# Optimization experiments

Measured on AMD Instinct MI355X. Metric: run time of the kernel, lower is better.

## Reference

```python
import jax, jax.numpy as jnp
import numpy as np

DEPTH = 4
HEADS = 8
DIM = 512
MLP = 2048
EPS = 1e-5


def layernorm(x, w, b):
    m = x.mean(-1, keepdims=True)
    v = x.var(-1, keepdims=True)
    return (x - m) * jax.lax.rsqrt(v + EPS) * w + b


def setup_inputs() -> dict:
    key = jax.random.key(0)
    ks = jax.random.split(key, 6)
    s = 0.02
    x = jax.random.normal(ks[0], (4, 2048, DIM), dtype=jnp.float32)
    return {
        "x": x,
        "ln1_w": jnp.ones((DEPTH, DIM), jnp.float32),
        "ln1_b": jnp.zeros((DEPTH, DIM), jnp.float32),
        "qkv_w": jax.random.normal(ks[1], (DEPTH, 3 * DIM, DIM), jnp.float32) * s,
        "proj_w": jax.random.normal(ks[2], (DEPTH, DIM, DIM), jnp.float32) * s,
        "proj_b": jnp.zeros((DEPTH, DIM), jnp.float32),
        "ln2_w": jnp.ones((DEPTH, DIM), jnp.float32),
        "ln2_b": jnp.zeros((DEPTH, DIM), jnp.float32),
        "fc1_w": jax.random.normal(ks[3], (DEPTH, MLP, DIM), jnp.float32) * s,
        "fc1_b": jnp.zeros((DEPTH, MLP), jnp.float32),
        "fc2_w": jax.random.normal(ks[4], (DEPTH, DIM, MLP), jnp.float32) * s,
        "fc2_b": jnp.zeros((DEPTH, DIM), jnp.float32),
    }


def reference(x, ln1_w, ln1_b, qkv_w, proj_w, proj_b, ln2_w, ln2_b, fc1_w, fc1_b, fc2_w, fc2_b):
    B, N, C = x.shape
    Dh = C // HEADS
    scale = Dh ** (-0.5)
    for i in range(DEPTH):
        # PreNorm attention block
        h = layernorm(x, ln1_w[i], ln1_b[i])
        qkv = (h @ qkv_w[i].T).reshape(B, N, 3, HEADS, Dh).transpose(2, 0, 3, 1, 4)
        q, k, v = qkv[0], qkv[1], qkv[2]          # [B,H,N,Dh]
        attn = jax.nn.softmax(jnp.einsum('bhnd,bhmd->bhnm', q, k) * scale, axis=-1)
        o = jnp.einsum('bhnm,bhmd->bhnd', attn, v).transpose(0, 2, 1, 3).reshape(B, N, C)
        x = o @ proj_w[i].T + proj_b[i] + x
        # PreNorm FFN block (exact erf GELU, matching torch nn.GELU default)
        h = layernorm(x, ln2_w[i], ln2_b[i])
        h = jax.nn.gelu(h @ fc1_w[i].T + fc1_b[i], approximate=False)
        x = h @ fc2_w[i].T + fc2_b[i] + x
    return x
```

## Files before the change

### kernel.cpp

```cpp
#include <hip/hip_runtime.h>
#include <hip/hip_bf16.h>
#include <math.h>

#define NB 4
#define HEADS 8
#define DIM 512
#define MLP 2048
#define NT 2048
#define DH 64
#define M_TOK (NB*NT)

typedef __bf16 bf16;
typedef __bf16 bf16x2 __attribute__((ext_vector_type(2)));
typedef __bf16 bf16x4 __attribute__((ext_vector_type(4)));
typedef __bf16 bf16x8 __attribute__((ext_vector_type(8)));
typedef float f32x4 __attribute__((ext_vector_type(4)));

__device__ __forceinline__ void gl_lds16(const void* g, void* l) {
    __builtin_amdgcn_global_load_lds((const __attribute__((address_space(1))) unsigned int*)g,
                                     (__attribute__((address_space(3))) unsigned int*)l, 16, 0, 0);
}

#define BARRIER() do { __builtin_amdgcn_s_barrier(); asm volatile("" ::: "memory"); } while(0)
#define WAIT_VM4() asm volatile("s_waitcnt vmcnt(4)" ::: "memory")
#define WAIT_VM0() asm volatile("s_waitcnt vmcnt(0)" ::: "memory")

__global__ void cvt_bf16_kernel(const float* __restrict__ src, bf16* __restrict__ dst, int n) {
    int i = (blockIdx.x * 256 + threadIdx.x) * 4;
    if (i < n) {
        float4 v = *(const float4*)(src + i);
        bf16x4 o;
        o[0] = (bf16)v.x; o[1] = (bf16)v.y; o[2] = (bf16)v.z; o[3] = (bf16)v.w;
        *(bf16x4*)(dst + i) = o;
    }
}

__global__ void ln_kernel(const float* __restrict__ X, const float* __restrict__ gam,
                          const float* __restrict__ bet, bf16* __restrict__ out) {
    int w = threadIdx.x >> 6, l = threadIdx.x & 63;
    long row = (long)blockIdx.x * 4 + w;
    const float* xp = X + row * DIM + l * 8;
    float4 a = *(const float4*)xp;
    float4 b = *(const float4*)(xp + 4);
    float s1 = a.x + a.y + a.z + a.w + b.x + b.y + b.z + b.w;
    float s2 = a.x*a.x + a.y*a.y + a.z*a.z + a.w*a.w + b.x*b.x + b.y*b.y + b.z*b.z + b.w*b.w;
#pragma unroll
    for (int off = 32; off; off >>= 1) { s1 += __shfl_xor(s1, off); s2 += __shfl_xor(s2, off); }
    float mean = s1 * (1.f / 512.f);
    float var  = s2 * (1.f / 512.f) - mean * mean;
    float rstd = rsqrtf(var + 1e-5f);
    float4 g0 = *(const float4*)(gam + l * 8), g1 = *(const float4*)(gam + l * 8 + 4);
    float4 b0 = *(const float4*)(bet + l * 8), b1 = *(const float4*)(bet + l * 8 + 4);
    bf16x8 o;
    o[0] = (bf16)((a.x - mean) * rstd * g0.x + b0.x);
    o[1] = (bf16)((a.y - mean) * rstd * g0.y + b0.y);
    o[2] = (bf16)((a.z - mean) * rstd * g0.z + b0.z);
    o[3] = (bf16)((a.w - mean) * rstd * g0.w + b0.w);
    o[4] = (bf16)((b.x - mean) * rstd * g1.x + b1.x);
    o[5] = (bf16)((b.y - mean) * rstd * g1.y + b1.y);
    o[6] = (bf16)((b.z - mean) * rstd * g1.z + b1.z);
    o[7] = (bf16)((b.w - mean) * rstd * g1.w + b1.w);
    *(bf16x8*)(out + row * DIM + l * 8) = o;
}

#define G_LOADA(AF, B_, MQ) do { \
  _Pragma("unroll") for (int mi_ = 0; mi_ < 2; ++mi_) \
  _Pragma("unroll") for (int kk_ = 0; kk_ < 2; ++kk_) { \
    int row_ = wr * 64 + ((MQ) * 2 + mi_) * 16 + c; \
    AF[mi_][kk_] = *(const bf16x8*)&Abuf[B_][row_ * 64 + (((kk_ * 64 + g * 16) ^ sw) >> 1)]; \
  } } while (0)

#define G_LOADB(BF, B_, NQ) do { \
  _Pragma("unroll") for (int ni_ = 0; ni_ < 2; ++ni_) \
  _Pragma("unroll") for (int kk_ = 0; kk_ < 2; ++kk_) { \
    int row_ = wc * 64 + ((NQ) * 2 + ni_) * 16 + c; \
    BF[ni_][kk_] = *(const bf16x8*)&Bbuf[B_][row_ * 64 + (((kk_ * 64 + g * 16) ^ sw) >> 1)]; \
  } } while (0)

#define G_MFMA(AF, BF, MQ, NQ) do { \
  __builtin_amdgcn_s_setprio(1); \
  _Pragma("unroll") for (int mi_ = 0; mi_ < 2; ++mi_) \
  _Pragma("unroll") for (int ni_ = 0; ni_ < 2; ++ni_) \
  _Pragma("unroll") for (int kk_ = 0; kk_ < 2; ++kk_) \
    acc[(MQ)*2+mi_][(NQ)*2+ni_] = __builtin_amdgcn_mfma_f32_16x16x32_bf16( \
        AF[mi_][kk_], BF[ni_][kk_], acc[(MQ)*2+mi_][(NQ)*2+ni_], 0, 0, 0); \
  __builtin_amdgcn_s_setprio(0); \
} while (0)

#define G_STAGE_A(J_, H_) do { int j_ = (J_); if (j_ < nkt) { \
  bf16* db_ = Abuf[j_ & 1]; const bf16* sb_ = Aptr + (size_t)j_ * 64 + coloff; \
  _Pragma("unroll") for (int q_ = 0; q_ < 2; ++q_) { \
    int rw_ = q_ * 64 + (H_) * 32 + (w << 3); \
    gl_lds16(sb_ + (size_t)(arow0 + rw_ + lr) * KN, db_ + rw_ * 64); \
  } } } while (0)

#define G_STAGE_B(J_, H_) do { int j_ = (J_); if (j_ < nkt) { \
  bf16* db_ = Bbuf[j_ & 1]; const bf16* sb_ = Wptr + (size_t)j_ * 64 + coloff; \
  _Pragma("unroll") for (int q_ = 0; q_ < 2; ++q_) { \
    int rw_ = q_ * 64 + (H_) * 32 + (w << 3); \
    gl_lds16(sb_ + (size_t)(bcol0 + rw_ + lr) * KN, db_ + rw_ * 64); \
  } } } while (0)

template<int EPI, int KN>
__global__ __launch_bounds__(256, 2) void gemm128(const bf16* __restrict__ Aptr,
                                                  const bf16* __restrict__ Wptr,
                                                  const float* __restrict__ bias,
                                                  const float* __restrict__ resid,
                                                  void* outp, int N, bf16* __restrict__ vtout) {
    __shared__ bf16 Abuf[2][128 * 64];
    __shared__ bf16 Bbuf[2][128 * 64];
    const int t = threadIdx.x, w = t >> 6, l = t & 63;
    const int wr = w >> 1, wc = w & 1, g = l >> 4, c = l & 15;
    const int sw = (c & 7) << 4;
    const int lr = l >> 3;
    const int coloff = ((l & 7) ^ lr) << 3;

    int nwg = gridDim.x, bid = blockIdx.x;
    int q8 = nwg >> 3, r8 = nwg & 7;
    int xcd = bid & 7, rank = bid >> 3;
    int swz = (xcd < r8) ? xcd * (q8 + 1) + rank : r8 * (q8 + 1) + (xcd - r8) * q8 + rank;
    int tiles_n = N >> 7;
    long arow0 = (long)(swz / tiles_n) * 128;
    long bcol0 = (long)(swz % tiles_n) * 128;

    const int nkt = KN / 64;
    const int niter = nkt / 2;
    f32x4 acc[4][4] = {};
    bf16x8 af[2][2], bn0[2][2], bn1[2][2];

    G_STAGE_A(0, 0); G_STAGE_B(0, 0); G_STAGE_A(0, 1); G_STAGE_B(0, 1);
    G_STAGE_A(1, 0); G_STAGE_B(1, 0);

#pragma unroll 1
    for (int tt = 0; tt < niter; ++tt) {
        const int J0 = 2 * tt, J1 = 2 * tt + 1;
        const bool last = (tt == niter - 1);
        WAIT_VM4(); BARRIER();
        G_LOADA(af, 0, 0); G_LOADB(bn0, 0, 0);
        G_STAGE_A(J0 + 1, 1);
        G_MFMA(af, bn0, 0, 0);
        BARRIER();
        G_LOADB(bn1, 0, 1);
        G_STAGE_B(J0 + 1, 1);
        G_MFMA(af, bn1, 0, 1);
        BARRIER();
        G_LOADA(af, 0, 1);
        G_STAGE_A(J0 + 2, 0);
        G_MFMA(af, bn0, 1, 0);
        BARRIER();
        G_STAGE_B(J0 + 2, 0);
        G_MFMA(af, bn1, 1, 1);
        BARRIER();
        if (last) { WAIT_VM0(); } else { WAIT_VM4(); }
        BARRIER();
        G_LOADA(af, 1, 0); G_LOADB(bn0, 1, 0);
        G_STAGE_A(J1 + 1, 1);
        G_MFMA(af, bn0, 0, 0);
        BARRIER();
        G_LOADB(bn1, 1, 1);
        G_STAGE_B(J1 + 1, 1);
        G_MFMA(af, bn1, 0, 1);
        BARRIER();
        G_LOADA(af, 1, 1);
        G_STAGE_A(J1 + 2, 0);
        G_MFMA(af, bn0, 1, 0);
        BARRIER();
        G_STAGE_B(J1 + 2, 0);
        G_MFMA(af, bn1, 1, 1);
        BARRIER();
    }

    if constexpr (EPI == 0) {
        const int s = (int)(bcol0 >> 9);
        const float qscale = 0.18033688011112042f;
        if (s == 2) {
#pragma unroll
            for (int m = 0; m < 4; ++m)
#pragma unroll
                for (int n = 0; n < 4; ++n) {
                    int col = (int)(bcol0 + wc * 64 + n * 16 + c);
                    int d = col & 63, hh = (col >> 6) & 7;
                    long row = arow0 + wr * 64 + m * 16 + g * 4;
                    int bb = (int)(row >> 11), nn = (int)(row & 2047);
                    bf16x4 o4;
#pragma unroll
                    for (int r = 0; r < 4; ++r) o4[r] = (bf16)acc[m][n][r];
                    *(bf16x4*)(vtout + ((long)(bb * 8 + hh) * 64 + d) * 2048 + nn) = o4;
                }
        } else {
            const float sc = (s == 0) ? qscale : 1.0f;
#pragma unroll
            for (int m = 0; m < 4; ++m)
#pragma unroll
                for (int n = 0; n < 4; ++n) {
                    int col = (int)(bcol0 + wc * 64 + n * 16 + c);
                    int hh = (col >> 6) & 7, d = col & 63;
                    long row = arow0 + wr * 64 + m * 16 + g * 4;
#pragma unroll
                    for (int r = 0; r < 4; ++r) {
                        long rr = row + r;
                        int bb = (int)(rr >> 11), nn = (int)(rr & 2047);
                        ((bf16*)outp)[(((long)(s * NB + bb) * HEADS + hh) * NT + nn) * DH + d] =
                            (bf16)(acc[m][n][r] * sc);
                    }
                }
        }
    }
}

template<int KN, int NOUT, int EPI>
__global__ __launch_bounds__(256, 2) void gemm_n64(const bf16* __restrict__ A,
                                                   const bf16* __restrict__ W,
                                                   const float* __restrict__ bias,
                                                   const float* __restrict__ resid,
                                                   void* __restrict__ outp) {
    __shared__ bf16 As[128 * 64];
    __shared__ bf16 Bs[64 * 64];
    const int t = threadIdx.x, w = t >> 6, l = t & 63;
    const int wr = w >> 1, wc = w & 1, g = l >> 4, c = l & 15;
    const long arow0 = (long)blockIdx.y * 128;
    const long bcol0 = (long)blockIdx.x * 64;
    f32x4 acc[4][2] = {};
    const int lrow = l >> 3, lcol = (l & 7) * 8;
    const bf16* Ab = A + (arow0 + lrow) * (long)KN + lcol;
    const bf16* Wb = W + (bcol0 + lrow) * (long)KN + lcol;
    for (int k0 = 0; k0 < KN; k0 += 64) {
#pragma unroll
        for (int q = 0; q < 4; ++q)
            gl_lds16(Ab + (long)(w * 4 + q) * 8 * KN + k0, &As[(w * 4 + q) * 512]);
#pragma unroll
        for (int q = 0; q < 2; ++q)
            gl_lds16(Wb + (long)(w * 2 + q) * 8 * KN + k0, &Bs[(w * 2 + q) * 512]);
        __syncthreads();
#pragma unroll
        for (int kk = 0; kk < 2; ++kk) {
            bf16x8 afv[4], bfr[2];
#pragma unroll
            for (int m = 0; m < 4; ++m)
                afv[m] = *(const bf16x8*)&As[(wr * 64 + m * 16 + c) * 64 + kk * 32 + g * 8];
#pragma unroll
            for (int n = 0; n < 2; ++n)
                bfr[n] = *(const bf16x8*)&Bs[(wc * 32 + n * 16 + c) * 64 + kk * 32 + g * 8];
#pragma unroll
            for (int m = 0; m < 4; ++m)
#pragma unroll
                for (int n = 0; n < 2; ++n)
                    acc[m][n] = __builtin_amdgcn_mfma_f32_16x16x32_bf16(afv[m], bfr[n], acc[m][n], 0, 0, 0);
        }
        __syncthreads();
    }
#pragma unroll
    for (int m = 0; m < 4; ++m)
#pragma unroll
        for (int n = 0; n < 2; ++n) {
            long row = arow0 + wr * 64 + m * 16 + g * 4;
            long col = bcol0 + wc * 32 + n * 16 + c;
#pragma unroll
            for (int r = 0; r < 4; ++r) {
                long rr = row + r;
                float v = acc[m][n][r] + bias[col];
                if constexpr (EPI == 1) {
                    ((float*)outp)[rr * NOUT + col] = v + resid[rr * NOUT + col];
                } else {
                    float ge = 0.5f * v * (1.f + erff(v * 0.70710678118654752f));
                    ((bf16*)outp)[rr * NOUT + col] = (bf16)ge;
                }
            }
        }
}

#define NKT (NT / 64)

#define ATT_BODY(BUF, KT) do { \
    __syncthreads(); \
    if ((KT) + 1 < NKT) { \
        const bf16* ks_ = kbase + (size_t)((KT) + 1) * (64 * DH); \
        const bf16* vs_ = vbase + ((KT) + 1) * 64; \
        gl_lds16(ks_,           &Ks[(BUF) ^ 1][(w * 8) * 64]); \
        gl_lds16(ks_ + 32 * DH, &Ks[(BUF) ^ 1][(32 + w * 8) * 64]); \
        gl_lds16(vs_,           &Vs[(BUF) ^ 1][(w * 8) * 64]); \
        gl_lds16(vs_ + 32 * NT, &Vs[(BUF) ^ 1][(32 + w * 8) * 64]); \
    } \
    const bf16* ksb = &Ks[BUF][0]; \
    const char* vsb = (const char*)&Vs[BUF][0]; \
    bf16x8 kf[4][2]; \
    _Pragma("unroll") for (int kc = 0; kc < 4; ++kc) \
    _Pragma("unroll") for (int kk = 0; kk < 2; ++kk) \
        kf[kc][kk] = *(const bf16x8*)&ksb[(kc * 16 + c) * 64 + (((kk * 64 + g * 16) ^ xr) >> 1)]; \
    f32x4 st[4] = {}; \
    _Pragma("unroll") for (int kc = 0; kc < 4; ++kc) \
    _Pragma("unroll") for (int kk = 0; kk < 2; ++kk) \
        st[kc] = __builtin_amdgcn_mfma_f32_16x16x32_bf16(kf[kc][kk], qf[kk], st[kc], 0, 0, 0); \
    bf16x8 vf[4][2]; \
    _Pragma("unroll") for (int dc = 0; dc < 4; ++dc) \
    _Pragma("unroll") for (int ks = 0; ks < 2; ++ks) \
        vf[dc][ks] = *(const bf16x8*)(vsb + (dc * 16 + c) * 128 + ((ks * 64 + g * 16) ^ xr)); \
    bf16x8 pf[2]; \
    _Pragma("unroll") for (int a = 0; a < 4; ++a) \
    _Pragma("unroll") for (int r = 0; r < 4; ++r) \
        pf[a >> 1][(a & 1) * 4 + r] = (bf16)exp2f(st[a][r]); \
    _Pragma("unroll") for (int ks = 0; ks < 2; ++ks) \
        sacc = __builtin_amdgcn_mfma_f32_16x16x32_bf16(ones8, pf[ks], sacc, 0, 0, 0); \
    _Pragma("unroll") for (int dc = 0; dc < 4; ++dc) \
    _Pragma("unroll") for (int ks = 0; ks < 2; ++ks) \
        oacc[dc] = __builtin_amdgcn_mfma_f32_16x16x32_bf16(vf[dc][ks], pf[ks], oacc[dc], 0, 0, 0); \
} while (0)

__global__ __launch_bounds__(256, 4) void attn_kernel(const bf16* __restrict__ qkv,
                                                      const bf16* __restrict__ vt,
                                                      bf16* __restrict__ O) {
    __shared__ bf16 Ks[2][64 * 64];
    __shared__ bf16 Vs[2][64 * 64];
    const int t = threadIdx.x, w = t >> 6, l = t & 63;
    const int g = l >> 4, c = l & 15;
    const int wg = blockIdx.x;
    const int xcd = wg & 7, rank = wg >> 3;
    const int bh = xcd + 8 * (rank >> 5);
    const int qt = rank & 31;
    const bf16* Qb = qkv + (long)bh * (NT * DH);
    const bf16* Kb = Qb + (long)(NB * HEADS) * (NT * DH);
    const bf16* Vtb = vt + (long)bh * (DH * NT);
    const int q0 = qt * 64 + w * 16;
    const int lr = l >> 3, lc = l & 7;
    const int sch = ((lc ^ lr) & 7) * 8;
    const int xr = (c & 7) << 4;

    const bf16* kbase = Kb + (long)(w * 8 + lr) * DH + sch;
    const bf16* vbase = Vtb + (long)(w * 8 + lr) * NT + sch;

    bf16x8 qf[2];
#pragma unroll
    for (int kk = 0; kk < 2; ++kk)
        qf[kk] = *(const bf16x8*)(Qb + (long)(q0 + c) * DH + kk * 32 + g * 8);

    bf16x8 ones8;
#pragma unroll
    for (int j = 0; j < 8; ++j) ones8[j] = (bf16)1.0f;

    f32x4 oacc[4] = {};
    f32x4 sacc = {};

    gl_lds16(kbase,           &Ks[0][(w * 8) * 64]);
    gl_lds16(kbase + 32 * DH, &Ks[0][(32 + w * 8) * 64]);
    gl_lds16(vbase,           &Vs[0][(w * 8) * 64]);
    gl_lds16(vbase + 32 * NT, &Vs[0][(32 + w * 8) * 64]);

#pragma unroll 1
    for (int kt2 = 0; kt2 < NKT / 2; ++kt2) {
        ATT_BODY(0, kt2 * 2);
        ATT_BODY(1, kt2 * 2 + 1);
    }

    float inv = 1.f / sacc[0];

    char* ol = (char*)&Ks[0][0] + w * 2048;
#pragma unroll
    for (int dc = 0; dc < 4; ++dc) {
        bf16x4 o4;
#pragma unroll
        for (int r = 0; r < 4; ++r) o4[r] = (bf16)(oacc[dc][r] * inv);
        *(bf16x4*)(ol + c * 128 + ((dc * 32 + g * 8) ^ xr)) = o4;
    }
    const int orow = l >> 2, oc = (l & 3) * 16;
    const int bb = bh >> 3, hh = bh & 7;
    long tok = (long)bb * NT + q0 + orow;
    bf16* og = O + tok * DIM + hh * 64 + oc;
    const int xr2 = (orow & 7) << 4;
    bf16x8 v0 = *(const bf16x8*)(ol + orow * 128 + ((oc * 2) ^ xr2));
    bf16x8 v1 = *(const bf16x8*)(ol + orow * 128 + ((oc * 2 + 16) ^ xr2));
    *(bf16x8*)og = v0;
    *(bf16x8*)(og + 8) = v1;
}

extern "C" void kernel_launch(void* const* d_in, const int* in_sizes, int n_in,
                              void* d_out, int out_size, void* d_ws, size_t ws_size,
                              hipStream_t stream) {
    const float* x      = (const float*)d_in[0];
    const float* ln1_w  = (const float*)d_in[1];
    const float* ln1_b  = (const float*)d_in[2];
    const float* qkv_w  = (const float*)d_in[3];
    const float* proj_w = (const float*)d_in[4];
    const float* proj_b = (const float*)d_in[5];
    const float* ln2_w  = (const float*)d_in[6];
    const float* ln2_b  = (const float*)d_in[7];
    const float* fc1_w  = (const float*)d_in[8];
    const float* fc1_b  = (const float*)d_in[9];
    const float* fc2_w  = (const float*)d_in[10];
    const float* fc2_b  = (const float*)d_in[11];
    float* X = (float*)d_out;

    char* ws = (char*)d_ws;
    bf16* h_bf   = (bf16*)(ws);
    bf16* scr_bf = (bf16*)(ws + (size_t)(8  << 20));
    bf16* vt_bf  = (bf16*)(ws + (size_t)(32 << 20));
    bf16* o_bf   = (bf16*)(ws + (size_t)(40 << 20));
    bf16* w_qkv  = (bf16*)(ws + (size_t)(48 << 20));
    bf16* w_proj = w_qkv  + (size_t)4 * 1536 * 512;
    bf16* w_fc1  = w_proj + (size_t)4 * 512 * 512;
    bf16* w_fc2  = w_fc1  + (size_t)4 * 2048 * 512;

    {
        int n;
        n = 4 * 1536 * 512; cvt_bf16_kernel<<<n / 1024, 256, 0, stream>>>(qkv_w,  w_qkv,  n);
        n = 4 * 512 * 512;  cvt_bf16_kernel<<<n / 1024, 256, 0, stream>>>(proj_w, w_proj, n);
        n = 4 * 2048 * 512; cvt_bf16_kernel<<<n / 1024, 256, 0, stream>>>(fc1_w,  w_fc1,  n);
        n = 4 * 512 * 2048; cvt_bf16_kernel<<<n / 1024, 256, 0, stream>>>(fc2_w,  w_fc2,  n);
    }
    hipMemcpyAsync(X, x, (size_t)M_TOK * DIM * sizeof(float), hipMemcpyDeviceToDevice, stream);

    for (int i = 0; i < 4; ++i) {
        ln_kernel<<<M_TOK / 4, 256, 0, stream>>>(X, ln1_w + i * 512, ln1_b + i * 512, h_bf);
        gemm128<0, 512><<<(M_TOK / 128) * (1536 / 128), 256, 0, stream>>>(
            h_bf, w_qkv + (size_t)i * 1536 * 512, nullptr, nullptr, scr_bf, 1536, vt_bf);
        attn_kernel<<<1024, 256, 0, stream>>>(scr_bf, vt_bf, o_bf);
        gemm_n64<512, 512, 1><<<dim3(8, 64), 256, 0, stream>>>(
            o_bf, w_proj + (size_t)i * 512 * 512, proj_b + i * 512, X, X);
        ln_kernel<<<M_TOK / 4, 256, 0, stream>>>(X, ln2_w + i * 512, ln2_b + i * 512, h_bf);
        gemm_n64<512, 2048, 2><<<dim3(32, 64), 256, 0, stream>>>(
            h_bf, w_fc1 + (size_t)i * 2048 * 512, fc1_b + i * 2048, nullptr, scr_bf);
        gemm_n64<2048, 512, 1><<<dim3(8, 64), 256, 0, stream>>>(
            scr_bf, w_fc2 + (size_t)i * 512 * 2048, fc2_b + i * 512, X, X);
    }
}
```

Baseline: 743.0 us.

## Software-pipeline attention QK, use 128-tile GEMM for fc1, drop input copy

The attention loop is restructured into a two-stage software pipeline. The QK^T MFMAs for the next key tile are issued alongside the PV MFMAs of the current tile under raised wave priority, and loads are prefetched two tiles ahead. The fc1 GEMM with GELU epilogue moves from the 64-wide kernel to the 128x128 gemm128 kernel through a new epilogue branch. The initial device-to-device copy of x is removed by reading x directly in the first layer. Register pressure rises in attention, and the larger fc1 tiles change occupancy.

```diff
diff --git a/kernel.cpp b/kernel.cpp
--- a/kernel.cpp
+++ b/kernel.cpp
@@ -205,6 +205,21 @@
                     }
                 }
         }
+    } else {
+#pragma unroll
+        for (int m = 0; m < 4; ++m)
+#pragma unroll
+            for (int n = 0; n < 4; ++n) {
+                long row = arow0 + wr * 64 + m * 16 + g * 4;
+                long col = bcol0 + wc * 64 + n * 16 + c;
+#pragma unroll
+                for (int r = 0; r < 4; ++r) {
+                    long rr = row + r;
+                    float u = acc[m][n][r] + bias[col];
+                    float ge = 0.5f * u * (1.f + erff(u * 0.70710678118654752f));
+                    ((bf16*)outp)[rr * N + col] = (bf16)ge;
+                }
+            }
     }
 }
 
@@ -271,39 +286,46 @@
 
 #define NKT (NT / 64)
 
-#define ATT_BODY(BUF, KT) do { \
-    __syncthreads(); \
-    if ((KT) + 1 < NKT) { \
-        const bf16* ks_ = kbase + (size_t)((KT) + 1) * (64 * DH); \
-        const bf16* vs_ = vbase + ((KT) + 1) * 64; \
-        gl_lds16(ks_,           &Ks[(BUF) ^ 1][(w * 8) * 64]); \
-        gl_lds16(ks_ + 32 * DH, &Ks[(BUF) ^ 1][(32 + w * 8) * 64]); \
-        gl_lds16(vs_,           &Vs[(BUF) ^ 1][(w * 8) * 64]); \
-        gl_lds16(vs_ + 32 * NT, &Vs[(BUF) ^ 1][(32 + w * 8) * 64]); \
-    } \
-    const bf16* ksb = &Ks[BUF][0]; \
-    const char* vsb = (const char*)&Vs[BUF][0]; \
-    bf16x8 kf[4][2]; \
+#define ATT_STAGE(J_, B_) do { \
+    const bf16* ks_ = kbase + (size_t)(J_) * (64 * DH); \
+    const bf16* vs_ = vbase + (J_) * 64; \
+    gl_lds16(ks_,           &Ks[B_][(w * 8) * 64]); \
+    gl_lds16(ks_ + 32 * DH, &Ks[B_][(32 + w * 8) * 64]); \
+    gl_lds16(vs_,           &Vs[B_][(w * 8) * 64]); \
+    gl_lds16(vs_ + 32 * NT, &Vs[B_][(32 + w * 8) * 64]); \
+} while (0)
+
+#define ATT_QK(B_, ST) do { \
+    bf16x8 kf_[4][2]; \
     _Pragma("unroll") for (int kc = 0; kc < 4; ++kc) \
     _Pragma("unroll") for (int kk = 0; kk < 2; ++kk) \
-        kf[kc][kk] = *(const bf16x8*)&ksb[(kc * 16 + c) * 64 + (((kk * 64 + g * 16) ^ xr) >> 1)]; \
-    f32x4 st[4] = {}; \
+        kf_[kc][kk] = *(const bf16x8*)&Ks[B_][(kc * 16 + c) * 64 + (((kk * 64 + g * 16) ^ xr) >> 1)]; \
     _Pragma("unroll") for (int kc = 0; kc < 4; ++kc) \
     _Pragma("unroll") for (int kk = 0; kk < 2; ++kk) \
-        st[kc] = __builtin_amdgcn_mfma_f32_16x16x32_bf16(kf[kc][kk], qf[kk], st[kc], 0, 0, 0); \
+        ST[kc] = __builtin_amdgcn_mfma_f32_16x16x32_bf16(kf_[kc][kk], qf[kk], ST[kc], 0, 0, 0); \
+} while (0)
+
+#define ATT_BODY(BUF, KT) do { \
     bf16x8 vf[4][2]; \
     _Pragma("unroll") for (int dc = 0; dc < 4; ++dc) \
     _Pragma("unroll") for (int ks = 0; ks < 2; ++ks) \
-        vf[dc][ks] = *(const bf16x8*)(vsb + (dc * 16 + c) * 128 + ((ks * 64 + g * 16) ^ xr)); \
+        vf[dc][ks] = *(const bf16x8*)((const char*)&Vs[BUF][0] + (dc * 16 + c) * 128 + ((ks * 64 + g * 16) ^ xr)); \
     bf16x8 pf[2]; \
     _Pragma("unroll") for (int a = 0; a < 4; ++a) \
     _Pragma("unroll") for (int r = 0; r < 4; ++r) \
         pf[a >> 1][(a & 1) * 4 + r] = (bf16)exp2f(st[a][r]); \
+    __syncthreads(); \
+    if ((KT) + 2 < NKT) ATT_STAGE((KT) + 2, BUF); \
+    f32x4 stn[4] = {}; \
+    __builtin_amdgcn_s_setprio(1); \
+    if ((KT) + 1 < NKT) ATT_QK((BUF) ^ 1, stn); \
     _Pragma("unroll") for (int ks = 0; ks < 2; ++ks) \
         sacc = __builtin_amdgcn_mfma_f32_16x16x32_bf16(ones8, pf[ks], sacc, 0, 0, 0); \
     _Pragma("unroll") for (int dc = 0; dc < 4; ++dc) \
     _Pragma("unroll") for (int ks = 0; ks < 2; ++ks) \
         oacc[dc] = __builtin_amdgcn_mfma_f32_16x16x32_bf16(vf[dc][ks], pf[ks], oacc[dc], 0, 0, 0); \
+    __builtin_amdgcn_s_setprio(0); \
+    _Pragma("unroll") for (int kc = 0; kc < 4; ++kc) st[kc] = stn[kc]; \
 } while (0)
 
 __global__ __launch_bounds__(256, 4) void attn_kernel(const bf16* __restrict__ qkv,
@@ -339,11 +361,12 @@
 
     f32x4 oacc[4] = {};
     f32x4 sacc = {};
-
-    gl_lds16(kbase,           &Ks[0][(w * 8) * 64]);
-    gl_lds16(kbase + 32 * DH, &Ks[0][(32 + w * 8) * 64]);
-    gl_lds16(vbase,           &Vs[0][(w * 8) * 64]);
-    gl_lds16(vbase + 32 * NT, &Vs[0][(32 + w * 8) * 64]);
+    f32x4 st[4] = {};
+
+    ATT_STAGE(0, 0);
+    ATT_STAGE(1, 1);
+    __syncthreads();
+    ATT_QK(0, st);
 
 #pragma unroll 1
     for (int kt2 = 0; kt2 < NKT / 2; ++kt2) {
@@ -361,6 +384,7 @@
         for (int r = 0; r < 4; ++r) o4[r] = (bf16)(oacc[dc][r] * inv);
         *(bf16x4*)(ol + c * 128 + ((dc * 32 + g * 8) ^ xr)) = o4;
     }
+    __builtin_amdgcn_s_waitcnt(0);
     const int orow = l >> 2, oc = (l & 3) * 16;
     const int bb = bh >> 3, hh = bh & 7;
     long tok = (long)bb * NT + q0 + orow;
@@ -406,18 +430,18 @@
         n = 4 * 2048 * 512; cvt_bf16_kernel<<<n / 1024, 256, 0, stream>>>(fc1_w,  w_fc1,  n);
         n = 4 * 512 * 2048; cvt_bf16_kernel<<<n / 1024, 256, 0, stream>>>(fc2_w,  w_fc2,  n);
     }
-    hipMemcpyAsync(X, x, (size_t)M_TOK * DIM * sizeof(float), hipMemcpyDeviceToDevice, stream);
 
     for (int i = 0; i < 4; ++i) {
-        ln_kernel<<<M_TOK / 4, 256, 0, stream>>>(X, ln1_w + i * 512, ln1_b + i * 512, h_bf);
+        const float* Xin = (i == 0) ? x : X;
+        ln_kernel<<<M_TOK / 4, 256, 0, stream>>>(Xin, ln1_w + i * 512, ln1_b + i * 512, h_bf);
         gemm128<0, 512><<<(M_TOK / 128) * (1536 / 128), 256, 0, stream>>>(
             h_bf, w_qkv + (size_t)i * 1536 * 512, nullptr, nullptr, scr_bf, 1536, vt_bf);
         attn_kernel<<<1024, 256, 0, stream>>>(scr_bf, vt_bf, o_bf);
         gemm_n64<512, 512, 1><<<dim3(8, 64), 256, 0, stream>>>(
-            o_bf, w_proj + (size_t)i * 512 * 512, proj_b + i * 512, X, X);
+            o_bf, w_proj + (size_t)i * 512 * 512, proj_b + i * 512, Xin, X);
         ln_kernel<<<M_TOK / 4, 256, 0, stream>>>(X, ln2_w + i * 512, ln2_b + i * 512, h_bf);
-        gemm_n64<512, 2048, 2><<<dim3(32, 64), 256, 0, stream>>>(
-            h_bf, w_fc1 + (size_t)i * 2048 * 512, fc1_b + i * 2048, nullptr, scr_bf);
+        gemm128<2, 512><<<(M_TOK / 128) * (2048 / 128), 256, 0, stream>>>(
+            h_bf, w_fc1 + (size_t)i * 2048 * 512, fc1_b + i * 2048, nullptr, scr_bf, 2048, nullptr);
         gemm_n64<2048, 512, 1><<<dim3(8, 64), 256, 0, stream>>>(
             scr_bf, w_fc2 + (size_t)i * 512 * 2048, fc2_b + i * 512, X, X);
     }
```

Measured after the change: 727.0 us. -2.2%, faster.
